# Kernel optimization log

Measured on AMD Instinct MI355X. Metric: run time of the kernel, lower is better.

The kernel has to match this reference:

```python
import jax, jax.numpy as jnp
import numpy as np

NUM_HEADS = 16


def setup_inputs() -> dict:
    key = jax.random.key(0)
    k1, k2, k3 = jax.random.split(key, 3)
    x = jax.random.normal(k1, (2, 2048, 1024), dtype=jnp.float32)
    w_qkv = jax.random.normal(k2, (3072, 1024), dtype=jnp.float32) * 0.02
    b_qkv = jax.random.normal(k3, (3072,), dtype=jnp.float32) * 0.02
    return {"x": x, "w_qkv": w_qkv, "b_qkv": b_qkv}


def reference(x, w_qkv, b_qkv):
    b, s, _ = x.shape
    d_model = w_qkv.shape[0] // 3
    head_dim = d_model // NUM_HEADS
    # fused QKV projection (torch Linear: x @ W^T + b)
    qkv = x @ w_qkv.T + b_qkv                      # [b, s, 3*d_model]
    qkv = qkv.reshape(b, s, NUM_HEADS, 3 * head_dim)
    qkv = jnp.transpose(qkv, (0, 2, 1, 3))          # [b, h, s, 3*hd]
    q, k, v = jnp.split(qkv, 3, axis=-1)            # each [b, h, s, hd]
    scale = 1.0 / np.sqrt(head_dim).astype(np.float32)
    scores = jnp.einsum("bhqd,bhkd->bhqk", q, k) * scale
    attn = jax.nn.softmax(scores, axis=-1)
    values = jnp.einsum("bhqk,bhkd->bhqd", attn, v)  # [b, h, s, hd]
    # Faithful to source: reshape WITHOUT permuting heads back (head-interleaved)
    return values.reshape(b, s, d_model)
```

## Files before the change

### kernel.cpp

```cpp
#include <hip/hip_runtime.h>
#include <cstdint>

typedef unsigned short ushort_t;

#define M_ROWS 4096
#define N_COLS 3072
#define K_DIM  1024
#define S_LEN  2048
#define NHEADS 16
#define HDIM   64
#define QSCALE 0.1803368801111204f

typedef __bf16 bf16_t;
typedef bf16_t  bf16x8  __attribute__((ext_vector_type(8)));
typedef short   shortx4 __attribute__((ext_vector_type(4)));
typedef float   floatx4 __attribute__((ext_vector_type(4)));
typedef ushort_t ushortx4 __attribute__((ext_vector_type(4)));

union U32x2S4 { unsigned u[2]; shortx4 s; };

__device__ __forceinline__ unsigned short f2bf(float f) {
  unsigned u = __float_as_uint(f);
  u += 0x7FFFu + ((u >> 16) & 1u);
  return (unsigned short)(u >> 16);
}

__device__ __forceinline__ unsigned pkbf(float a, float b) {
  unsigned ua = __float_as_uint(a) + 0x8000u;
  unsigned ub = __float_as_uint(b) + 0x8000u;
  return __builtin_amdgcn_perm(ub, ua, 0x07060302u);
}

__device__ __forceinline__ unsigned cvtpk(float a, float b) {
#if __has_builtin(__builtin_amdgcn_cvt_pk_bf16_f32)
  auto t = __builtin_amdgcn_cvt_pk_bf16_f32(a, b);
  unsigned r;
  __builtin_memcpy(&r, &t, 4);
  return r;
#else
  return pkbf(a, b);
#endif
}

__device__ __forceinline__ float fexp2(float x) {
#if __has_builtin(__builtin_amdgcn_exp2f)
  return __builtin_amdgcn_exp2f(x);
#else
  float r; asm volatile("v_exp_f32 %0, %1\n\ts_nop 1" : "=v"(r) : "v"(x)); return r;
#endif
}

__device__ __forceinline__ void gload_lds16(const void* g, void* l) {
  __builtin_amdgcn_global_load_lds(
      (const __attribute__((address_space(1))) unsigned int*)g,
      (__attribute__((address_space(3))) unsigned int*)l,
      16, 0, 0);
}

__global__ __launch_bounds__(256) void cvt_bf16_kernel(
    const float* __restrict__ x, const float* __restrict__ w,
    ushort_t* __restrict__ Xb, ushort_t* __restrict__ Wb) {
  const int NX8 = (M_ROWS * K_DIM) / 8;
  int i = blockIdx.x * 256 + threadIdx.x;
  const float4* src;
  ushort_t* dst;
  int idx;
  if (i < NX8) { src = (const float4*)x; dst = Xb; idx = i; }
  else         { src = (const float4*)w; dst = Wb; idx = i - NX8; }
  float4 a = src[2 * idx];
  float4 b = src[2 * idx + 1];
  uint4 o;
  o.x = cvtpk(a.x, a.y);
  o.y = cvtpk(a.z, a.w);
  o.z = cvtpk(b.x, b.y);
  o.w = cvtpk(b.z, b.w);
  *(uint4*)(dst + 8 * (size_t)idx) = o;
}

__global__ __launch_bounds__(256) void qkv_gemm_kernel(
    const ushort_t* __restrict__ Xb, const ushort_t* __restrict__ Wb,
    const float* __restrict__ bias,
    ushort_t* __restrict__ Qb, ushort_t* __restrict__ Kb, ushort_t* __restrict__ Vb) {
  __shared__ ushort_t As[128 * 64];
  __shared__ ushort_t Bs[128 * 64];
  const int tid = threadIdx.x;
  const int l = tid & 63, w = tid >> 6;
  const int quad = l >> 4, lj = l & 15;
  const int m0 = blockIdx.y * 128, n0 = blockIdx.x * 128;
  const int wm = (w & 1) * 64, wn = (w >> 1) * 64;

  floatx4 acc[4][4] = {};

  const int srow = w * 32 + (l >> 3);
  const int scol = ((l & 7) ^ (l >> 3)) * 8;
  const ushort_t* gA = Xb + (size_t)(m0 + srow) * K_DIM + scol;
  const ushort_t* gB = Wb + (size_t)(n0 + srow) * K_DIM + scol;
  ushort_t* lA = As + (w * 32) * 64;
  ushort_t* lB = Bs + (w * 32) * 64;

  const int swr = lj & 7;

  for (int k0 = 0; k0 < K_DIM; k0 += 64) {
    __syncthreads();
#pragma unroll
    for (int c = 0; c < 4; ++c) {
      gload_lds16(gA + (size_t)(c * 8) * K_DIM + k0, lA + c * 8 * 64);
      gload_lds16(gB + (size_t)(c * 8) * K_DIM + k0, lB + c * 8 * 64);
    }
    __syncthreads();
#pragma unroll
    for (int kk = 0; kk < 2; ++kk) {
      const int ch = ((kk * 4 + quad) ^ swr) * 8;
      bf16x8 aF[4], bF[4];
#pragma unroll
      for (int i = 0; i < 4; ++i)
        aF[i] = *(const bf16x8*)(As + (wm + i * 16 + lj) * 64 + ch);
#pragma unroll
      for (int j = 0; j < 4; ++j)
        bF[j] = *(const bf16x8*)(Bs + (wn + j * 16 + lj) * 64 + ch);
#pragma unroll
      for (int i = 0; i < 4; ++i)
#pragma unroll
        for (int j = 0; j < 4; ++j)
          acc[i][j] = __builtin_amdgcn_mfma_f32_16x16x32_bf16(aF[i], bF[j], acc[i][j], 0, 0, 0);
    }
  }

#pragma unroll
  for (int j = 0; j < 4; ++j) {
    const int n = n0 + wn + j * 16 + lj;
    const int h = n / 192;
    const int r = n - h * 192;
    const int seg = r >> 6;
    const int d = r & 63;
    const float bv = bias[n];
    ushort_t* dst = (seg == 0) ? Qb : (seg == 1) ? Kb : Vb;
    const float scl = (seg == 0) ? QSCALE : 1.0f;
    const size_t base = (size_t)h * S_LEN * HDIM + d;
#pragma unroll
    for (int i = 0; i < 4; ++i) {
#pragma unroll
      for (int rg = 0; rg < 4; ++rg) {
        const int m = m0 + wm + i * 16 + quad * 4 + rg;
        const int bi = m >> 11;
        const int si = m & 2047;
        dst[base + ((size_t)bi * NHEADS * S_LEN + si) * HDIM] =
            f2bf((acc[i][j][rg] + bv) * scl);
      }
    }
  }
}

__global__ __launch_bounds__(512, 4) void attn_kernel(
    const ushort_t* __restrict__ Qb, const ushort_t* __restrict__ Kb,
    const ushort_t* __restrict__ Vb, float* __restrict__ out) {
  __shared__ ushort_t Ks[128 * 64];
  __shared__ ushort_t Vs[64 * 140];
  const int tid = threadIdx.x;
  const int l = tid & 63, w = tid >> 6;
  const int quad = l >> 4, lj = l & 15;
  const int id = (blockIdx.x & 7) * 64 + (blockIdx.x >> 3);
  const int bh = id >> 4;
  const int qt = id & 15;
  const int q0 = qt * 128 + w * 16;
  const size_t headoff = (size_t)bh * S_LEN * HDIM;

  bf16x8 qF[2];
#pragma unroll
  for (int kk = 0; kk < 2; ++kk)
    qF[kk] = *(const bf16x8*)(Qb + headoff + (size_t)(q0 + lj) * HDIM +
                              kk * 32 + quad * 8);

  floatx4 accO[4] = {};
  float l_runA = 0.f, l_runB = 0.f;

  const int kr = tid >> 3;
  const int kc = ((tid & 7) ^ (kr & 7)) * 8;
  const ushort_t* gK = Kb + headoff + (size_t)kr * HDIM + kc;
  ushort_t* lK = Ks + tid * 8;

  const int dq = tid & 15;
  const int spw = tid >> 4;
  const ushort_t* gV = Vb + headoff + dq * 4;
  unsigned* Vs32 = (unsigned*)Vs;
  const int swz = (dq >> 2) << 1;

  const int swk = lj & 7;

  for (int kb = 0; kb < 16; ++kb) {
    const int kv0 = kb * 128;
    __syncthreads();
#pragma unroll
    for (int c = 0; c < 2; ++c)
      gload_lds16(gK + (size_t)(kv0 + c * 64) * HDIM, lK + c * 64 * 64);
#pragma unroll
    for (int R = 0; R < 2; ++R) {
      const int sp = R * 32 + spw;
      const ushort_t* g = gV + (size_t)(kv0 + 2 * sp) * HDIM;
      const uint2 v0 = *(const uint2*)g;
      const uint2 v1 = *(const uint2*)(g + HDIM);
      unsigned o0 = __builtin_amdgcn_perm(v1.x, v0.x, 0x05040100u);
      unsigned o1 = __builtin_amdgcn_perm(v1.x, v0.x, 0x07060302u);
      unsigned o2 = __builtin_amdgcn_perm(v1.y, v0.y, 0x05040100u);
      unsigned o3 = __builtin_amdgcn_perm(v1.y, v0.y, 0x07060302u);
      const int sp2 = sp ^ swz;
      Vs32[(4 * dq + 0) * 70 + sp2] = o0;
      Vs32[(4 * dq + 1) * 70 + sp2] = o1;
      Vs32[(4 * dq + 2) * 70 + sp2] = o2;
      Vs32[(4 * dq + 3) * 70 + sp2] = o3;
    }
    __syncthreads();

    __builtin_amdgcn_s_setprio(1);
    floatx4 accST[8];
#pragma unroll
    for (int c = 0; c < 8; ++c) {
      const ushort_t* krow = Ks + (c * 16 + lj) * 64;
      bf16x8 kF0 = *(const bf16x8*)(krow + ((quad ^ swk) * 8));
      bf16x8 kF1 = *(const bf16x8*)(krow + (((quad ^ swk) ^ 4) * 8));
      floatx4 z = {0.f, 0.f, 0.f, 0.f};
      z = __builtin_amdgcn_mfma_f32_16x16x32_bf16(kF0, qF[0], z, 0, 0, 0);
      accST[c] = __builtin_amdgcn_mfma_f32_16x16x32_bf16(kF1, qF[1], z, 0, 0, 0);
    }
    __builtin_amdgcn_s_setprio(0);

    shortx4 aP[8];
    float lsA = 0.f, lsB = 0.f;
#pragma unroll
    for (int c = 0; c < 8; ++c) {
      float p0 = fexp2(accST[c][0]);
      float p1 = fexp2(accST[c][1]);
      float p2 = fexp2(accST[c][2]);
      float p3 = fexp2(accST[c][3]);
      lsA += p0 + p1;
      lsB += p2 + p3;
      U32x2S4 t;
      t.u[0] = cvtpk(p0, p1);
      t.u[1] = cvtpk(p2, p3);
      aP[c] = t.s;
    }
    l_runA += lsA;
    l_runB += lsB;

    __builtin_amdgcn_s_setprio(1);
#pragma unroll
    for (int dt = 0; dt < 4; ++dt) {
      const ushort_t* vp = Vs + (dt * 16 + lj) * 140 + (quad ^ dt) * 4;
#pragma unroll
      for (int c = 0; c < 8; ++c) {
        shortx4 vF = *(const shortx4*)(vp + c * 16);
        accO[dt] = __builtin_amdgcn_mfma_f32_16x16x16bf16_1k(aP[c], vF, accO[dt], 0, 0, 0);
      }
    }
    __builtin_amdgcn_s_setprio(0);
  }

  {
    float ls = l_runA + l_runB;
    ls += __shfl_xor(ls, 16, 64);
    ls += __shfl_xor(ls, 32, 64);
    const float inv = 1.0f / ls;
    const int sbase = (l & 48) | (quad * 4);
    float iv[4];
    iv[0] = __shfl(inv, sbase + 0, 64);
    iv[1] = __shfl(inv, sbase + 1, 64);
    iv[2] = __shfl(inv, sbase + 2, 64);
    iv[3] = __shfl(inv, sbase + 3, 64);
#pragma unroll
    for (int dt = 0; dt < 4; ++dt) {
#pragma unroll
      for (int rg = 0; rg < 4; ++rg) {
        const int q = q0 + quad * 4 + rg;
        out[headoff + (size_t)q * HDIM + dt * 16 + lj] = accO[dt][rg] * iv[rg];
      }
    }
  }
}

extern "C" void kernel_launch(void* const* d_in, const int* in_sizes, int n_in,
                              void* d_out, int out_size, void* d_ws, size_t ws_size,
                              hipStream_t stream) {
  (void)in_sizes; (void)n_in; (void)out_size; (void)ws_size;
  const float* x  = (const float*)d_in[0];
  const float* wq = (const float*)d_in[1];
  const float* bq = (const float*)d_in[2];
  float* out = (float*)d_out;

  char* ws = (char*)d_ws;
  ushort_t* Qb = (ushort_t*)(ws);
  ushort_t* Kb = (ushort_t*)(ws + 8388608);
  ushort_t* Vb = (ushort_t*)(ws + 16777216);
  ushort_t* Xb = (ushort_t*)(ws + 25165824);
  ushort_t* Wb = (ushort_t*)(ws + 33554432);

  cvt_bf16_kernel<<<3584, 256, 0, stream>>>(x, wq, Xb, Wb);
  qkv_gemm_kernel<<<dim3(N_COLS / 128, M_ROWS / 128), 256, 0, stream>>>(Xb, Wb, bq, Qb, Kb, Vb);
  attn_kernel<<<512, 512, 0, stream>>>(Qb, Kb, Vb, out);
}
```

Baseline: 163.9 us.

## Double-buffer K/V tiles in LDS to overlap loads with attention compute

The attention kernel now keeps two LDS buffers for the K and V tiles. It prefetches the next tile's K (via direct global-to-LDS loads) and V (via registers, permuted and stored after the softmax) while computing on the current tile, which leaves one barrier per iteration instead of two. The s_setprio priority hints around the MFMA sections are removed. LDS use per block roughly doubles, to about 68KB, so the four-blocks-per-CU launch bound may no longer fit and occupancy could drop.

```diff
diff --git a/kernel.cpp b/kernel.cpp
--- a/kernel.cpp
+++ b/kernel.cpp
@@ -154,8 +154,8 @@
 __global__ __launch_bounds__(512, 4) void attn_kernel(
     const ushort_t* __restrict__ Qb, const ushort_t* __restrict__ Kb,
     const ushort_t* __restrict__ Vb, float* __restrict__ out) {
-  __shared__ ushort_t Ks[128 * 64];
-  __shared__ ushort_t Vs[64 * 140];
+  __shared__ ushort_t Ks[2][128 * 64];
+  __shared__ ushort_t Vs[2][64 * 140];
   const int tid = threadIdx.x;
   const int l = tid & 63, w = tid >> 6;
   const int quad = l >> 4, lj = l & 15;
@@ -177,52 +177,72 @@
   const int kr = tid >> 3;
   const int kc = ((tid & 7) ^ (kr & 7)) * 8;
   const ushort_t* gK = Kb + headoff + (size_t)kr * HDIM + kc;
-  ushort_t* lK = Ks + tid * 8;
 
   const int dq = tid & 15;
   const int spw = tid >> 4;
   const ushort_t* gV = Vb + headoff + dq * 4;
-  unsigned* Vs32 = (unsigned*)Vs;
   const int swz = (dq >> 2) << 1;
 
   const int swk = lj & 7;
 
-  for (int kb = 0; kb < 16; ++kb) {
-    const int kv0 = kb * 128;
-    __syncthreads();
+  {
+    uint2 va[2], vb[2];
+#pragma unroll
+    for (int R = 0; R < 2; ++R) {
+      const ushort_t* g = gV + (size_t)(2 * (R * 32 + spw)) * HDIM;
+      va[R] = *(const uint2*)g;
+      vb[R] = *(const uint2*)(g + HDIM);
+    }
 #pragma unroll
     for (int c = 0; c < 2; ++c)
-      gload_lds16(gK + (size_t)(kv0 + c * 64) * HDIM, lK + c * 64 * 64);
+      gload_lds16(gK + (size_t)(c * 64) * HDIM, &Ks[0][0] + tid * 8 + c * 64 * 64);
+    unsigned* vdst = (unsigned*)&Vs[0][0];
 #pragma unroll
     for (int R = 0; R < 2; ++R) {
       const int sp = R * 32 + spw;
-      const ushort_t* g = gV + (size_t)(kv0 + 2 * sp) * HDIM;
-      const uint2 v0 = *(const uint2*)g;
-      const uint2 v1 = *(const uint2*)(g + HDIM);
-      unsigned o0 = __builtin_amdgcn_perm(v1.x, v0.x, 0x05040100u);
-      unsigned o1 = __builtin_amdgcn_perm(v1.x, v0.x, 0x07060302u);
-      unsigned o2 = __builtin_amdgcn_perm(v1.y, v0.y, 0x05040100u);
-      unsigned o3 = __builtin_amdgcn_perm(v1.y, v0.y, 0x07060302u);
+      unsigned o0 = __builtin_amdgcn_perm(vb[R].x, va[R].x, 0x05040100u);
+      unsigned o1 = __builtin_amdgcn_perm(vb[R].x, va[R].x, 0x07060302u);
+      unsigned o2 = __builtin_amdgcn_perm(vb[R].y, va[R].y, 0x05040100u);
+      unsigned o3 = __builtin_amdgcn_perm(vb[R].y, va[R].y, 0x07060302u);
       const int sp2 = sp ^ swz;
-      Vs32[(4 * dq + 0) * 70 + sp2] = o0;
-      Vs32[(4 * dq + 1) * 70 + sp2] = o1;
-      Vs32[(4 * dq + 2) * 70 + sp2] = o2;
-      Vs32[(4 * dq + 3) * 70 + sp2] = o3;
-    }
-    __syncthreads();
-
-    __builtin_amdgcn_s_setprio(1);
+      vdst[(4 * dq + 0) * 70 + sp2] = o0;
+      vdst[(4 * dq + 1) * 70 + sp2] = o1;
+      vdst[(4 * dq + 2) * 70 + sp2] = o2;
+      vdst[(4 * dq + 3) * 70 + sp2] = o3;
+    }
+  }
+  __syncthreads();
+
+  for (int kb = 0; kb < 16; ++kb) {
+    const int cur = kb & 1;
+    const ushort_t* Kc = &Ks[cur][0];
+    const ushort_t* Vc = &Vs[cur][0];
+
+    uint2 va[2], vb[2];
+    if (kb < 15) {
+      const int kv1 = (kb + 1) * 128;
+#pragma unroll
+      for (int R = 0; R < 2; ++R) {
+        const ushort_t* g = gV + (size_t)(kv1 + 2 * (R * 32 + spw)) * HDIM;
+        va[R] = *(const uint2*)g;
+        vb[R] = *(const uint2*)(g + HDIM);
+      }
+#pragma unroll
+      for (int c = 0; c < 2; ++c)
+        gload_lds16(gK + (size_t)(kv1 + c * 64) * HDIM,
+                    &Ks[cur ^ 1][0] + tid * 8 + c * 64 * 64);
+    }
+
     floatx4 accST[8];
 #pragma unroll
     for (int c = 0; c < 8; ++c) {
-      const ushort_t* krow = Ks + (c * 16 + lj) * 64;
+      const ushort_t* krow = Kc + (c * 16 + lj) * 64;
       bf16x8 kF0 = *(const bf16x8*)(krow + ((quad ^ swk) * 8));
       bf16x8 kF1 = *(const bf16x8*)(krow + (((quad ^ swk) ^ 4) * 8));
       floatx4 z = {0.f, 0.f, 0.f, 0.f};
       z = __builtin_amdgcn_mfma_f32_16x16x32_bf16(kF0, qF[0], z, 0, 0, 0);
       accST[c] = __builtin_amdgcn_mfma_f32_16x16x32_bf16(kF1, qF[1], z, 0, 0, 0);
     }
-    __builtin_amdgcn_s_setprio(0);
 
     shortx4 aP[8];
     float lsA = 0.f, lsB = 0.f;
@@ -242,17 +262,34 @@
     l_runA += lsA;
     l_runB += lsB;
 
-    __builtin_amdgcn_s_setprio(1);
+    if (kb < 15) {
+      unsigned* vdst = (unsigned*)&Vs[cur ^ 1][0];
+#pragma unroll
+      for (int R = 0; R < 2; ++R) {
+        const int sp = R * 32 + spw;
+        unsigned o0 = __builtin_amdgcn_perm(vb[R].x, va[R].x, 0x05040100u);
+        unsigned o1 = __builtin_amdgcn_perm(vb[R].x, va[R].x, 0x07060302u);
+        unsigned o2 = __builtin_amdgcn_perm(vb[R].y, va[R].y, 0x05040100u);
+        unsigned o3 = __builtin_amdgcn_perm(vb[R].y, va[R].y, 0x07060302u);
+        const int sp2 = sp ^ swz;
+        vdst[(4 * dq + 0) * 70 + sp2] = o0;
+        vdst[(4 * dq + 1) * 70 + sp2] = o1;
+        vdst[(4 * dq + 2) * 70 + sp2] = o2;
+        vdst[(4 * dq + 3) * 70 + sp2] = o3;
+      }
+    }
+
 #pragma unroll
     for (int dt = 0; dt < 4; ++dt) {
-      const ushort_t* vp = Vs + (dt * 16 + lj) * 140 + (quad ^ dt) * 4;
+      const ushort_t* vp = Vc + (dt * 16 + lj) * 140 + (quad ^ dt) * 4;
 #pragma unroll
       for (int c = 0; c < 8; ++c) {
         shortx4 vF = *(const shortx4*)(vp + c * 16);
         accO[dt] = __builtin_amdgcn_mfma_f32_16x16x16bf16_1k(aP[c], vF, accO[dt], 0, 0, 0);
       }
     }
-    __builtin_amdgcn_s_setprio(0);
+
+    __syncthreads();
   }
 
   {
```

New measurement: 162.8 us, median of 3. About the same (-0.7%).
